# Kernel optimization log

Hardware: AMD Instinct MI355X
Metric: run time of the kernel (lower is better)

## Reference

```python
import jax, jax.numpy as jnp
import numpy as np

B, S, H = 4, 2048, 2048
E, K = 4, 2
FF = 4 * H  # standard MLP expert expansion


def setup_inputs() -> dict:
    key = jax.random.key(0)
    ks = jax.random.split(key, 5)
    sc = 0.02
    return {
        "hidden_states": jax.random.normal(ks[0], (B, S, H), jnp.float32),
        "w_gate": jax.random.normal(ks[1], (H, E), jnp.float32) * sc,
        "b_gate": jnp.zeros((E,), jnp.float32),
        "w1": jax.random.normal(ks[2], (E, H, FF), jnp.float32) * sc,
        "b1": jnp.zeros((E, FF), jnp.float32),
        "w2": jax.random.normal(ks[3], (E, FF, H), jnp.float32) * sc,
        "b2": jnp.zeros((E, H), jnp.float32),
    }


def reference(hidden_states, w_gate, b_gate, w1, b1, w2, b2):
    # Router: linear gate -> softmax -> top-k, renormalized gate weights
    logits = jnp.einsum("bsh,he->bse", hidden_states, w_gate) + b_gate
    probs = jax.nn.softmax(logits, axis=-1)                       # [B,S,E]
    top_p, top_i = jax.lax.top_k(probs, K)                        # [B,S,K]
    gate_w = top_p / jnp.sum(top_p, axis=-1, keepdims=True)

    # Switch-style load-balancing aux loss
    route = jax.nn.one_hot(top_i, E, dtype=probs.dtype)           # [B,S,K,E]
    frac_tokens = jnp.mean(jnp.sum(route, axis=2) / K, axis=(0, 1))  # [E]
    mean_prob = jnp.mean(probs, axis=(0, 1))                      # [E]
    aux_loss = E * jnp.sum(frac_tokens * mean_prob)

    # Dispatch/combine: small fixed expert count -> loop over experts,
    # dense FFN on all tokens, mask via gate weight (0 for unrouted tokens).
    out = jnp.zeros_like(hidden_states)
    for e in range(E):
        w_e = jnp.sum(gate_w * (top_i == e), axis=-1)             # [B,S]
        h = jax.nn.gelu(jnp.einsum("bsh,hf->bsf", hidden_states, w1[e]) + b1[e])
        y = jnp.einsum("bsf,fh->bsh", h, w2[e]) + b2[e]
        out = out + w_e[..., None] * y
    return out, aux_loss
```

## Files before the change

kernel.cpp:

```cpp
#include <hip/hip_runtime.h>

typedef unsigned short u16;
typedef __attribute__((ext_vector_type(8))) short bf16x8;
typedef __attribute__((ext_vector_type(4))) float f32x4;

#define TOK  8192
#define HD   2048
#define FFD  8192
#define NEXP 4

__device__ __forceinline__ u16 f2bf(float f){
  unsigned u = __float_as_uint(f);
  u += 0x7fffu + ((u >> 16) & 1u);
  return (u16)(u >> 16);
}

__device__ __forceinline__ float gelu_tanh(float x){
  float u = 0.7978845608028654f * (x + 0.044715f * x * x * x);
  return 0.5f * x * (1.0f + tanhf(u));
}

__device__ __forceinline__ void gload_lds16(const void* g, void* l){
  __builtin_amdgcn_global_load_lds((const __attribute__((address_space(1))) void*)g,
                                   (__attribute__((address_space(3))) void*)l, 16, 0, 0);
}

__device__ __forceinline__ f32x4 mfma_bf16(bf16x8 a, bf16x8 b, f32x4 c){
  asm("v_mfma_f32_16x16x32_bf16 %0, %1, %2, %0" : "+v"(c) : "v"(a), "v"(b));
  return c;
}

__global__ __launch_bounds__(256) void cvt_to_bf16(const float* __restrict__ in,
                                                   u16* __restrict__ out, int n4){
  int i = blockIdx.x * 256 + threadIdx.x;
  if (i >= n4) return;
  float4 v = ((const float4*)in)[i];
  ushort4 o;
  o.x = f2bf(v.x); o.y = f2bf(v.y); o.z = f2bf(v.z); o.w = f2bf(v.w);
  ((ushort4*)out)[i] = o;
}

__global__ __launch_bounds__(256) void transpose_cvt(const float* __restrict__ in,
                                                     u16* __restrict__ out, int R, int C){
  __shared__ float tile[64][65];
  int tx = threadIdx.x & 63;
  int ty = threadIdx.x >> 6;
  size_t r0 = (size_t)blockIdx.y * 64;
  size_t c0 = (size_t)blockIdx.x * 64;
  #pragma unroll
  for (int i = ty; i < 64; i += 4)
    tile[i][tx] = in[(r0 + i) * C + (c0 + tx)];
  __syncthreads();
  #pragma unroll
  for (int i = ty; i < 64; i += 4)
    out[(c0 + i) * R + (r0 + tx)] = f2bf(tile[tx][i]);
}

__global__ __launch_bounds__(256) void router_kernel(
    const float* __restrict__ X, const float* __restrict__ wg, const float* __restrict__ bg,
    float* __restrict__ probs, int* __restrict__ topi, float* __restrict__ gatew){
  int t = blockIdx.x;
  const float* x = X + (size_t)t * HD;
  float a0 = 0.f, a1 = 0.f, a2 = 0.f, a3 = 0.f;
  for (int h = threadIdx.x; h < HD; h += 256){
    float xv = x[h];
    float4 w = ((const float4*)wg)[h];
    a0 += xv * w.x; a1 += xv * w.y; a2 += xv * w.z; a3 += xv * w.w;
  }
  __shared__ float red[4][256];
  red[0][threadIdx.x] = a0; red[1][threadIdx.x] = a1;
  red[2][threadIdx.x] = a2; red[3][threadIdx.x] = a3;
  __syncthreads();
  for (int s = 128; s > 0; s >>= 1){
    if (threadIdx.x < (unsigned)s){
      #pragma unroll
      for (int e = 0; e < 4; e++) red[e][threadIdx.x] += red[e][threadIdx.x + s];
    }
    __syncthreads();
  }
  if (threadIdx.x == 0){
    float l[4], p[4];
    #pragma unroll
    for (int e = 0; e < 4; e++) l[e] = red[e][0] + bg[e];
    float mx = fmaxf(fmaxf(l[0], l[1]), fmaxf(l[2], l[3]));
    float s = 0.f;
    #pragma unroll
    for (int e = 0; e < 4; e++){ p[e] = expf(l[e] - mx); s += p[e]; }
    #pragma unroll
    for (int e = 0; e < 4; e++){ p[e] /= s; probs[t * 4 + e] = p[e]; }
    int e0 = 0;
    for (int e = 1; e < 4; e++) if (p[e] > p[e0]) e0 = e;
    int e1 = -1;
    for (int e = 0; e < 4; e++){ if (e == e0) continue; if (e1 < 0 || p[e] > p[e1]) e1 = e; }
    float g = p[e0] + p[e1];
    topi[t * 2] = e0; topi[t * 2 + 1] = e1;
    #pragma unroll
    for (int e = 0; e < 4; e++)
      gatew[(size_t)e * TOK + t] = (e == e0) ? p[e0] / g : (e == e1) ? p[e1] / g : 0.f;
  }
}

__global__ __launch_bounds__(256) void build_lists(const int* __restrict__ topi,
                                                   int* __restrict__ cnt,
                                                   int* __restrict__ lists){
  int t = blockIdx.x * 256 + threadIdx.x;
  if (t >= TOK) return;
  #pragma unroll
  for (int k = 0; k < 2; k++){
    int e = topi[t * 2 + k];
    int p = atomicAdd(cnt + e, 1);
    lists[e * TOK + p] = t;
  }
}

__global__ __launch_bounds__(256) void aux_kernel(const float* __restrict__ probs,
                                                  const int* __restrict__ topi,
                                                  float* __restrict__ out_aux){
  __shared__ float sp[4][256];
  __shared__ float sc[4][256];
  float p[4] = {0,0,0,0}, c[4] = {0,0,0,0};
  for (int t = threadIdx.x; t < TOK; t += 256){
    #pragma unroll
    for (int e = 0; e < 4; e++) p[e] += probs[t * 4 + e];
    c[topi[t * 2]]     += 1.f;
    c[topi[t * 2 + 1]] += 1.f;
  }
  #pragma unroll
  for (int e = 0; e < 4; e++){ sp[e][threadIdx.x] = p[e]; sc[e][threadIdx.x] = c[e]; }
  __syncthreads();
  for (int s = 128; s > 0; s >>= 1){
    if (threadIdx.x < (unsigned)s){
      #pragma unroll
      for (int e = 0; e < 4; e++){
        sp[e][threadIdx.x] += sp[e][threadIdx.x + s];
        sc[e][threadIdx.x] += sc[e][threadIdx.x + s];
      }
    }
    __syncthreads();
  }
  if (threadIdx.x == 0){
    float aux = 0.f;
    #pragma unroll
    for (int e = 0; e < 4; e++)
      aux += (sc[e][0] / (float)(TOK * 2)) * (sp[e][0] / (float)TOK);
    *out_aux = 4.f * aux;
  }
}

#define BM 128
#define BN 128
#define BK 64

template<int EPI>
__global__ __launch_bounds__(256) void gemm_moe(
    const u16* __restrict__ A, const u16* __restrict__ BT,
    const int* __restrict__ rowidx, const int* __restrict__ cntp,
    int m0, int N, int K,
    const float* __restrict__ bias,
    u16* __restrict__ Hout,
    const float* __restrict__ gate,
    float* __restrict__ Cout){
  const int Mv = *cntp;
  const int browg = m0 + blockIdx.y * BM;
  if (browg >= Mv) return;

  __shared__ __align__(16) u16 As[BM * BK];
  __shared__ __align__(16) u16 Bs[BN * BK];

  const int tid  = threadIdx.x;
  const int lane = tid & 63;
  const int wid  = tid >> 6;
  const int wr   = wid >> 1;
  const int wc   = wid & 1;
  const size_t bcol = (size_t)blockIdx.x * BN;

  const int srow = lane >> 3;
  const int scol = (lane & 7) * 8;
  const int r = lane & 15;
  const int h = lane >> 4;

  const u16* aptr[4];
  const u16* bptr[4];
  #pragma unroll
  for (int i = 0; i < 4; i++){
    const int c = wid * 4 + i;
    const int rr = browg + c * 8 + srow;
    int ar;
    if (EPI == 0){
      const int cr = rr < Mv ? rr : Mv - 1;
      ar = rowidx[cr];
    } else {
      ar = rr - m0;
    }
    aptr[i] = A + (size_t)ar * K + scol;
    bptr[i] = BT + (bcol + c * 8 + srow) * (size_t)K + scol;
  }

  f32x4 acc[4][4];
  #pragma unroll
  for (int m = 0; m < 4; m++)
    #pragma unroll
    for (int n = 0; n < 4; n++) acc[m][n] = (f32x4){0.f, 0.f, 0.f, 0.f};

  for (int kt = 0; kt < K; kt += BK){
    __syncthreads();
    #pragma unroll
    for (int i = 0; i < 4; i++){
      const int c = wid * 4 + i;
      gload_lds16(aptr[i] + kt, (char*)As + c * 1024);
      gload_lds16(bptr[i] + kt, (char*)Bs + c * 1024);
    }
    __syncthreads();
    #pragma unroll
    for (int kk = 0; kk < BK; kk += 32){
      bf16x8 av[4], bv[4];
      #pragma unroll
      for (int m = 0; m < 4; m++)
        av[m] = *(const bf16x8*)(As + (wr * 64 + m * 16 + r) * BK + kk + h * 8);
      #pragma unroll
      for (int n = 0; n < 4; n++)
        bv[n] = *(const bf16x8*)(Bs + (wc * 64 + n * 16 + r) * BK + kk + h * 8);
      #pragma unroll
      for (int m = 0; m < 4; m++)
        #pragma unroll
        for (int n = 0; n < 4; n++)
          acc[m][n] = mfma_bf16(av[m], bv[n], acc[m][n]);
    }
  }

  const int cl = lane & 15;
  const int rg = (lane >> 4) * 4;
  const size_t c0 = bcol + (size_t)wc * 64;
  float bvs[4];
  #pragma unroll
  for (int n = 0; n < 4; n++) bvs[n] = bias[c0 + n * 16 + cl];

  #pragma unroll
  for (int m = 0; m < 4; m++){
    const int rowg = browg + wr * 64 + m * 16 + rg;
    if (EPI == 0){
      const size_t rowl = (size_t)(rowg - m0);
      #pragma unroll
      for (int n = 0; n < 4; n++){
        const size_t col = c0 + n * 16 + cl;
        #pragma unroll
        for (int j = 0; j < 4; j++){
          float y = acc[m][n][j] + bvs[n];
          Hout[(rowl + j) * (size_t)N + col] = f2bf(gelu_tanh(y));
        }
      }
    } else {
      int   tok[4];
      float gv[4];
      #pragma unroll
      for (int j = 0; j < 4; j++){
        const bool v = (rowg + j) < Mv;
        tok[j] = v ? rowidx[rowg + j] : -1;
        gv[j]  = v ? gate[tok[j]] : 0.f;
      }
      #pragma unroll
      for (int n = 0; n < 4; n++){
        const size_t col = c0 + n * 16 + cl;
        #pragma unroll
        for (int j = 0; j < 4; j++){
          if (tok[j] >= 0){
            float y = acc[m][n][j] + bvs[n];
            const size_t idx = (size_t)tok[j] * N + col;
            Cout[idx] += gv[j] * y;
          }
        }
      }
    }
  }
}

extern "C" void kernel_launch(void* const* d_in, const int* in_sizes, int n_in,
                              void* d_out, int out_size, void* d_ws, size_t ws_size,
                              hipStream_t stream){
  const float* X  = (const float*)d_in[0];
  const float* wg = (const float*)d_in[1];
  const float* bg = (const float*)d_in[2];
  const float* w1 = (const float*)d_in[3];
  const float* b1 = (const float*)d_in[4];
  const float* w2 = (const float*)d_in[5];
  const float* b2 = (const float*)d_in[6];
  float* out = (float*)d_out;

  char* ws = (char*)d_ws;
  size_t off = 0;
  auto alloc = [&](size_t b) -> char* {
    char* p = ws + off;
    off = (off + b + 255) & ~(size_t)255;
    return p;
  };
  u16*   Xb    = (u16*)  alloc((size_t)TOK * HD * 2);
  u16*   W1T   = (u16*)  alloc((size_t)FFD * HD * 2);
  u16*   W2T   = (u16*)  alloc((size_t)HD * FFD * 2);
  float* probs = (float*)alloc((size_t)TOK * 4 * 4);
  int*   topi  = (int*)  alloc((size_t)TOK * 2 * 4);
  float* gatew = (float*)alloc((size_t)NEXP * TOK * 4);
  int*   cnt   = (int*)  alloc((size_t)NEXP * 4);
  int*   lists = (int*)  alloc((size_t)NEXP * TOK * 4);
  size_t remain = (ws_size > off) ? (ws_size - off) : 0;
  size_t ch = remain / ((size_t)FFD * 2);
  ch = (ch / 128) * 128;
  if (ch > TOK) ch = TOK;
  if (ch < 128) ch = 128;
  u16* Hb = (u16*)alloc(ch * (size_t)FFD * 2);

  hipMemsetAsync(cnt, 0, NEXP * sizeof(int), stream);
  hipMemsetAsync(out, 0, (size_t)TOK * HD * sizeof(float), stream);

  cvt_to_bf16<<<(TOK * HD / 4 + 255) / 256, 256, 0, stream>>>(X, Xb, TOK * HD / 4);
  router_kernel<<<TOK, 256, 0, stream>>>(X, wg, bg, probs, topi, gatew);
  build_lists<<<TOK / 256, 256, 0, stream>>>(topi, cnt, lists);
  aux_kernel<<<1, 256, 0, stream>>>(probs, topi, out + (out_size - 1));

  for (int e = 0; e < NEXP; ++e){
    transpose_cvt<<<dim3(FFD / 64, HD / 64), 256, 0, stream>>>(
        w1 + (size_t)e * HD * FFD, W1T, HD, FFD);
    transpose_cvt<<<dim3(HD / 64, FFD / 64), 256, 0, stream>>>(
        w2 + (size_t)e * FFD * HD, W2T, FFD, HD);
    for (int m0 = 0; m0 < TOK; m0 += (int)ch){
      gemm_moe<0><<<dim3(FFD / 128, (unsigned)(ch / 128)), 256, 0, stream>>>(
          Xb, W1T, lists + e * TOK, cnt + e, m0, FFD, HD,
          b1 + (size_t)e * FFD, Hb, nullptr, nullptr);
      gemm_moe<1><<<dim3(HD / 128, (unsigned)(ch / 128)), 256, 0, stream>>>(
          Hb, W2T, lists + e * TOK, cnt + e, m0, HD, FFD,
          b2 + (size_t)e * HD, nullptr,
          gatew + (size_t)e * TOK, out);
    }
  }
}
```

Before: 1.955 ms.

## Replace MoE GEMMs with 8-wave double-buffered swizzled 256-row tile kernels

Both expert GEMMs are rewritten as 512-thread kernels with 256-row tiles, double-buffered LDS, and an XOR-swizzled LDS layout. The next K-tile is loaded asynchronously in quarters while MFMAs run, paced by explicit vmcnt waits, barriers and setprio. Workgroup indices are remapped so neighbouring tiles land on the same XCD, which should improve cache reuse. The chunked M loop is replaced by a fixed per-expert capacity (CAPE=4608 rows). Tokens beyond that capacity would be silently dropped if routing were strongly imbalanced.

Measured after the change: 2.263 ms. 15.8% more time.

```diff
diff --git a/kernel.cpp b/kernel.cpp
--- a/kernel.cpp
+++ b/kernel.cpp
@@ -8,6 +8,10 @@
 #define HD   2048
 #define FFD  8192
 #define NEXP 4
+#define CAPE 4608
+
+#define S_BARRIER() asm volatile("s_barrier" ::: "memory")
+#define VMCNT(n)    asm volatile("s_waitcnt vmcnt(" #n ")" ::: "memory")
 
 __device__ __forceinline__ u16 f2bf(float f){
   unsigned u = __float_as_uint(f);
@@ -147,53 +151,166 @@
   }
 }
 
-#define BM 128
-#define BN 128
-#define BK 64
-
-template<int EPI>
-__global__ __launch_bounds__(256) void gemm_moe(
-    const u16* __restrict__ A, const u16* __restrict__ BT,
+__global__ __launch_bounds__(512, 2) void gemm1_8p(
+    const u16* __restrict__ Xb, const u16* __restrict__ BT,
     const int* __restrict__ rowidx, const int* __restrict__ cntp,
-    int m0, int N, int K,
-    const float* __restrict__ bias,
-    u16* __restrict__ Hout,
-    const float* __restrict__ gate,
-    float* __restrict__ Cout){
+    const float* __restrict__ bias, u16* __restrict__ Hout)
+{
+  __shared__ __align__(16) u16 As[2 * 256 * 64];
+  __shared__ __align__(16) u16 Bs[2 * 256 * 64];
   const int Mv = *cntp;
-  const int browg = m0 + blockIdx.y * BM;
+  const int nwg = gridDim.x * gridDim.y;
+  const int orig = blockIdx.x + gridDim.x * blockIdx.y;
+  const int q8 = nwg >> 3, r8 = nwg & 7, xcd = orig & 7, rank = orig >> 3;
+  const int v = (xcd < r8 ? xcd * (q8 + 1) : r8 * (q8 + 1) + (xcd - r8) * q8) + rank;
+  const int by = v % (int)gridDim.y, bx = v / (int)gridDim.y;
+  const int browg = by * 256;
   if (browg >= Mv) return;
-
-  __shared__ __align__(16) u16 As[BM * BK];
-  __shared__ __align__(16) u16 Bs[BN * BK];
-
-  const int tid  = threadIdx.x;
-  const int lane = tid & 63;
-  const int wid  = tid >> 6;
-  const int wr   = wid >> 1;
-  const int wc   = wid & 1;
-  const size_t bcol = (size_t)blockIdx.x * BN;
-
-  const int srow = lane >> 3;
-  const int scol = (lane & 7) * 8;
-  const int r = lane & 15;
-  const int h = lane >> 4;
-
-  const u16* aptr[4];
-  const u16* bptr[4];
-  #pragma unroll
-  for (int i = 0; i < 4; i++){
-    const int c = wid * 4 + i;
-    const int rr = browg + c * 8 + srow;
-    int ar;
-    if (EPI == 0){
-      const int cr = rr < Mv ? rr : Mv - 1;
-      ar = rowidx[cr];
-    } else {
-      ar = rr - m0;
-    }
-    aptr[i] = A + (size_t)ar * K + scol;
-    bptr[i] = BT + (bcol + c * 8 + srow) * (size_t)K + scol;
+  const size_t bcol = (size_t)bx * 256;
+
+  const int tid = threadIdx.x, lane = tid & 63, w = tid >> 6;
+  const int wr = w >> 2, wc = w & 3;
+  const int l8 = lane >> 3;
+  const int csw  = ((lane & 7) ^ l8) * 8;
+  const int sw   = (lane & 7) * 8;
+  const int h8   = ((lane >> 4) & 3) * 8;
+  const int colk0 = h8 ^ sw, colk1 = (32 | h8) ^ sw;
+  const int r16 = lane & 15;
+
+  const u16* bsrc[4]; int bch[4];
+  #pragma unroll
+  for (int j = 0; j < 4; j++){
+    int rb = wc * 64 + wr * 32 + j * 8;
+    bch[j] = rb * 128;
+    bsrc[j] = BT + (bcol + rb + l8) * (size_t)HD + csw;
+  }
+  const u16* asrc[4]; int ach[4];
+  #pragma unroll
+  for (int q = 0; q < 4; q++){
+    int rb = wr * 128 + q * 32 + wc * 8;
+    ach[q] = rb * 128;
+    int rl = browg + rb + l8; if (rl > Mv - 1) rl = Mv - 1;
+    asrc[q] = Xb + (size_t)rowidx[rl] * HD + csw;
+  }
+
+  f32x4 acc[8][4];
+  #pragma unroll
+  for (int m = 0; m < 8; m++)
+    #pragma unroll
+    for (int n = 0; n < 4; n++) acc[m][n] = (f32x4){0.f, 0.f, 0.f, 0.f};
+  bf16x8 bC[8];
+
+  const int NT = HD / 64;
+  #pragma unroll
+  for (int j = 0; j < 4; j++) gload_lds16(bsrc[j], (char*)Bs + bch[j]);
+  #pragma unroll
+  for (int q = 0; q < 4; q++) gload_lds16(asrc[q], (char*)As + ach[q]);
+  VMCNT(3); S_BARRIER();
+
+  for (int t = 0; t < NT; ++t){
+    const u16* asb = As + (t & 1) * 16384;
+    const u16* bsb = Bs + (t & 1) * 16384;
+    char* anb = (char*)As + ((t & 1) ^ 1) * 32768;
+    char* bnb = (char*)Bs + ((t & 1) ^ 1) * 32768;
+    const size_t ko = (size_t)(t + 1) * 64;
+    const bool lastT = (t == NT - 1);
+    #pragma unroll 4
+    for (int p = 0; p < 4; p++){
+      if (p == 0){
+        #pragma unroll
+        for (int nf = 0; nf < 4; nf++){
+          const u16* bp = bsb + (wc * 64 + nf * 16 + r16) * 64;
+          bC[nf * 2]     = *(const bf16x8*)(bp + colk0);
+          bC[nf * 2 + 1] = *(const bf16x8*)(bp + colk1);
+        }
+      }
+      bf16x8 a[2][2];
+      #pragma unroll
+      for (int mi = 0; mi < 2; mi++){
+        const u16* ap = asb + (wr * 128 + (2 * p + mi) * 16 + r16) * 64;
+        a[mi][0] = *(const bf16x8*)(ap + colk0);
+        a[mi][1] = *(const bf16x8*)(ap + colk1);
+      }
+      if (!lastT){
+        if      (p == 0){ gload_lds16(bsrc[0] + ko, bnb + bch[0]); gload_lds16(bsrc[1] + ko, bnb + bch[1]); }
+        else if (p == 1){ gload_lds16(bsrc[2] + ko, bnb + bch[2]); gload_lds16(bsrc[3] + ko, bnb + bch[3]); }
+        else if (p == 2){ gload_lds16(asrc[0] + ko, anb + ach[0]); gload_lds16(asrc[1] + ko, anb + ach[1]); }
+        else            { gload_lds16(asrc[2] + ko, anb + ach[2]); gload_lds16(asrc[3] + ko, anb + ach[3]); }
+      }
+      S_BARRIER();
+      __builtin_amdgcn_s_setprio(1);
+      #pragma unroll
+      for (int mi = 0; mi < 2; mi++)
+        #pragma unroll
+        for (int nf = 0; nf < 4; nf++){
+          acc[2 * p + mi][nf] = mfma_bf16(a[mi][0], bC[nf * 2],     acc[2 * p + mi][nf]);
+          acc[2 * p + mi][nf] = mfma_bf16(a[mi][1], bC[nf * 2 + 1], acc[2 * p + mi][nf]);
+        }
+      __builtin_amdgcn_s_setprio(0);
+      if (!lastT){ if (p == 0) VMCNT(4); else if (p == 1) VMCNT(5); else if (p == 2) VMCNT(6); else VMCNT(3); }
+      else       { if (p == 0) VMCNT(2); else if (p == 1) VMCNT(1); else if (p == 2) VMCNT(0); }
+      S_BARRIER();
+    }
+  }
+
+  const int cl = r16, rg = (lane >> 4) * 4;
+  const size_t c0 = bcol + wc * 64;
+  float bv[4];
+  #pragma unroll
+  for (int nf = 0; nf < 4; nf++) bv[nf] = bias[c0 + nf * 16 + cl];
+  #pragma unroll
+  for (int mf = 0; mf < 8; mf++){
+    const size_t rb = (size_t)(browg + wr * 128 + mf * 16 + rg);
+    #pragma unroll
+    for (int nf = 0; nf < 4; nf++){
+      const size_t col = c0 + nf * 16 + cl;
+      #pragma unroll
+      for (int j = 0; j < 4; j++)
+        Hout[(rb + j) * FFD + col] = f2bf(gelu_tanh(acc[mf][nf][j] + bv[nf]));
+    }
+  }
+}
+
+__global__ __launch_bounds__(512, 2) void gemm2_8p(
+    const u16* __restrict__ Hb, const u16* __restrict__ BT,
+    const int* __restrict__ rowidx, const int* __restrict__ cntp,
+    const float* __restrict__ bias, const float* __restrict__ gate,
+    float* __restrict__ Cout)
+{
+  __shared__ __align__(16) u16 As[2 * 256 * 64];
+  __shared__ __align__(16) u16 Bs[2 * 128 * 64];
+  const int Mv = *cntp;
+  const int nwg = gridDim.x * gridDim.y;
+  const int orig = blockIdx.x + gridDim.x * blockIdx.y;
+  const int q8 = nwg >> 3, r8 = nwg & 7, xcd = orig & 7, rank = orig >> 3;
+  const int v = (xcd < r8 ? xcd * (q8 + 1) : r8 * (q8 + 1) + (xcd - r8) * q8) + rank;
+  const int by = v % (int)gridDim.y, bx = v / (int)gridDim.y;
+  const int browg = by * 256;
+  if (browg >= Mv) return;
+  const size_t bcol = (size_t)bx * 128;
+
+  const int tid = threadIdx.x, lane = tid & 63, w = tid >> 6;
+  const int wr = w >> 1, wc = w & 1;
+  const int l8 = lane >> 3;
+  const int csw  = ((lane & 7) ^ l8) * 8;
+  const int sw   = (lane & 7) * 8;
+  const int h8   = ((lane >> 4) & 3) * 8;
+  const int colk0 = h8 ^ sw, colk1 = (32 | h8) ^ sw;
+  const int r16 = lane & 15;
+
+  const u16* bsrc[2]; int bch[2];
+  #pragma unroll
+  for (int j = 0; j < 2; j++){
+    int rb = wc * 64 + wr * 16 + j * 8;
+    bch[j] = rb * 128;
+    bsrc[j] = BT + (bcol + rb + l8) * (size_t)FFD + csw;
+  }
+  const u16* asrc[4]; int ach[4];
+  #pragma unroll
+  for (int q = 0; q < 4; q++){
+    int rb = wr * 64 + q * 16 + wc * 8;
+    ach[q] = rb * 128;
+    asrc[q] = Hb + (size_t)(browg + rb + l8) * FFD + csw;
   }
 
   f32x4 acc[4][4];
@@ -201,73 +318,80 @@
   for (int m = 0; m < 4; m++)
     #pragma unroll
     for (int n = 0; n < 4; n++) acc[m][n] = (f32x4){0.f, 0.f, 0.f, 0.f};
-
-  for (int kt = 0; kt < K; kt += BK){
-    __syncthreads();
-    #pragma unroll
-    for (int i = 0; i < 4; i++){
-      const int c = wid * 4 + i;
-      gload_lds16(aptr[i] + kt, (char*)As + c * 1024);
-      gload_lds16(bptr[i] + kt, (char*)Bs + c * 1024);
-    }
-    __syncthreads();
-    #pragma unroll
-    for (int kk = 0; kk < BK; kk += 32){
-      bf16x8 av[4], bv[4];
-      #pragma unroll
-      for (int m = 0; m < 4; m++)
-        av[m] = *(const bf16x8*)(As + (wr * 64 + m * 16 + r) * BK + kk + h * 8);
-      #pragma unroll
-      for (int n = 0; n < 4; n++)
-        bv[n] = *(const bf16x8*)(Bs + (wc * 64 + n * 16 + r) * BK + kk + h * 8);
-      #pragma unroll
-      for (int m = 0; m < 4; m++)
+  bf16x8 bC[8];
+
+  const int NT = FFD / 64;
+  gload_lds16(bsrc[0], (char*)Bs + bch[0]);
+  gload_lds16(bsrc[1], (char*)Bs + bch[1]);
+  #pragma unroll
+  for (int q = 0; q < 4; q++) gload_lds16(asrc[q], (char*)As + ach[q]);
+  VMCNT(3); S_BARRIER();
+
+  for (int t = 0; t < NT; ++t){
+    const u16* asb = As + (t & 1) * 16384;
+    const u16* bsb = Bs + (t & 1) * 8192;
+    char* anb = (char*)As + ((t & 1) ^ 1) * 32768;
+    char* bnb = (char*)Bs + ((t & 1) ^ 1) * 16384;
+    const size_t ko = (size_t)(t + 1) * 64;
+    const bool lastT = (t == NT - 1);
+    #pragma unroll 4
+    for (int p = 0; p < 4; p++){
+      if (p == 0){
         #pragma unroll
-        for (int n = 0; n < 4; n++)
-          acc[m][n] = mfma_bf16(av[m], bv[n], acc[m][n]);
-    }
-  }
-
-  const int cl = lane & 15;
-  const int rg = (lane >> 4) * 4;
-  const size_t c0 = bcol + (size_t)wc * 64;
-  float bvs[4];
-  #pragma unroll
-  for (int n = 0; n < 4; n++) bvs[n] = bias[c0 + n * 16 + cl];
-
-  #pragma unroll
-  for (int m = 0; m < 4; m++){
-    const int rowg = browg + wr * 64 + m * 16 + rg;
-    if (EPI == 0){
-      const size_t rowl = (size_t)(rowg - m0);
-      #pragma unroll
-      for (int n = 0; n < 4; n++){
-        const size_t col = c0 + n * 16 + cl;
-        #pragma unroll
-        for (int j = 0; j < 4; j++){
-          float y = acc[m][n][j] + bvs[n];
-          Hout[(rowl + j) * (size_t)N + col] = f2bf(gelu_tanh(y));
+        for (int nf = 0; nf < 4; nf++){
+          const u16* bp = bsb + (wc * 64 + nf * 16 + r16) * 64;
+          bC[nf * 2]     = *(const bf16x8*)(bp + colk0);
+          bC[nf * 2 + 1] = *(const bf16x8*)(bp + colk1);
         }
       }
-    } else {
-      int   tok[4];
-      float gv[4];
+      bf16x8 a0, a1;
+      {
+        const u16* ap = asb + (wr * 64 + p * 16 + r16) * 64;
+        a0 = *(const bf16x8*)(ap + colk0);
+        a1 = *(const bf16x8*)(ap + colk1);
+      }
+      if (!lastT){
+        if      (p == 0){ gload_lds16(bsrc[0] + ko, bnb + bch[0]); gload_lds16(bsrc[1] + ko, bnb + bch[1]); }
+        else if (p == 1){ gload_lds16(asrc[0] + ko, anb + ach[0]); gload_lds16(asrc[1] + ko, anb + ach[1]); }
+        else if (p == 2){ gload_lds16(asrc[2] + ko, anb + ach[2]); gload_lds16(asrc[3] + ko, anb + ach[3]); }
+      }
+      S_BARRIER();
+      __builtin_amdgcn_s_setprio(1);
+      #pragma unroll
+      for (int nf = 0; nf < 4; nf++){
+        acc[p][nf] = mfma_bf16(a0, bC[nf * 2],     acc[p][nf]);
+        acc[p][nf] = mfma_bf16(a1, bC[nf * 2 + 1], acc[p][nf]);
+      }
+      __builtin_amdgcn_s_setprio(0);
+      if (!lastT){ if (p == 0) VMCNT(4); else if (p == 1) VMCNT(5); else if (p == 2) VMCNT(6); else VMCNT(3); }
+      else       { if (p == 0) VMCNT(2); else if (p == 1) VMCNT(1); else if (p == 2) VMCNT(0); }
+      S_BARRIER();
+    }
+  }
+
+  const int cl = r16, rg = (lane >> 4) * 4;
+  const size_t c0 = bcol + wc * 64;
+  float bv[4];
+  #pragma unroll
+  for (int nf = 0; nf < 4; nf++) bv[nf] = bias[c0 + nf * 16 + cl];
+  #pragma unroll
+  for (int mf = 0; mf < 4; mf++){
+    const int rbase = browg + wr * 64 + mf * 16 + rg;
+    int   tok[4]; float gv[4];
+    #pragma unroll
+    for (int j = 0; j < 4; j++){
+      const bool ok = (rbase + j) < Mv;
+      tok[j] = ok ? rowidx[rbase + j] : -1;
+      gv[j]  = ok ? gate[tok[j]] : 0.f;
+    }
+    #pragma unroll
+    for (int nf = 0; nf < 4; nf++){
+      const size_t col = c0 + nf * 16 + cl;
       #pragma unroll
       for (int j = 0; j < 4; j++){
-        const bool v = (rowg + j) < Mv;
-        tok[j] = v ? rowidx[rowg + j] : -1;
-        gv[j]  = v ? gate[tok[j]] : 0.f;
-      }
-      #pragma unroll
-      for (int n = 0; n < 4; n++){
-        const size_t col = c0 + n * 16 + cl;
-        #pragma unroll
-        for (int j = 0; j < 4; j++){
-          if (tok[j] >= 0){
-            float y = acc[m][n][j] + bvs[n];
-            const size_t idx = (size_t)tok[j] * N + col;
-            Cout[idx] += gv[j] * y;
-          }
+        if (tok[j] >= 0){
+          const size_t idx = (size_t)tok[j] * HD + col;
+          Cout[idx] += gv[j] * (acc[mf][nf][j] + bv[nf]);
         }
       }
     }
@@ -277,6 +401,7 @@
 extern "C" void kernel_launch(void* const* d_in, const int* in_sizes, int n_in,
                               void* d_out, int out_size, void* d_ws, size_t ws_size,
                               hipStream_t stream){
+  (void)in_sizes; (void)n_in; (void)ws_size;
   const float* X  = (const float*)d_in[0];
   const float* wg = (const float*)d_in[1];
   const float* bg = (const float*)d_in[2];
@@ -301,12 +426,7 @@
   float* gatew = (float*)alloc((size_t)NEXP * TOK * 4);
   int*   cnt   = (int*)  alloc((size_t)NEXP * 4);
   int*   lists = (int*)  alloc((size_t)NEXP * TOK * 4);
-  size_t remain = (ws_size > off) ? (ws_size - off) : 0;
-  size_t ch = remain / ((size_t)FFD * 2);
-  ch = (ch / 128) * 128;
-  if (ch > TOK) ch = TOK;
-  if (ch < 128) ch = 128;
-  u16* Hb = (u16*)alloc(ch * (size_t)FFD * 2);
+  u16*   Hb    = (u16*)  alloc((size_t)CAPE * FFD * 2);
 
   hipMemsetAsync(cnt, 0, NEXP * sizeof(int), stream);
   hipMemsetAsync(out, 0, (size_t)TOK * HD * sizeof(float), stream);
@@ -321,14 +441,10 @@
         w1 + (size_t)e * HD * FFD, W1T, HD, FFD);
     transpose_cvt<<<dim3(HD / 64, FFD / 64), 256, 0, stream>>>(
         w2 + (size_t)e * FFD * HD, W2T, FFD, HD);
-    for (int m0 = 0; m0 < TOK; m0 += (int)ch){
-      gemm_moe<0><<<dim3(FFD / 128, (unsigned)(ch / 128)), 256, 0, stream>>>(
-          Xb, W1T, lists + e * TOK, cnt + e, m0, FFD, HD,
-          b1 + (size_t)e * FFD, Hb, nullptr, nullptr);
-      gemm_moe<1><<<dim3(HD / 128, (unsigned)(ch / 128)), 256, 0, stream>>>(
-          Hb, W2T, lists + e * TOK, cnt + e, m0, HD, FFD,
-          b2 + (size_t)e * HD, nullptr,
-          gatew + (size_t)e * TOK, out);
-    }
-  }
-}
+    gemm1_8p<<<dim3(FFD / 256, CAPE / 256), 512, 0, stream>>>(
+        Xb, W1T, lists + e * TOK, cnt + e, b1 + (size_t)e * FFD, Hb);
+    gemm2_8p<<<dim3(HD / 128, CAPE / 256), 512, 0, stream>>>(
+        Hb, W2T, lists + e * TOK, cnt + e, b2 + (size_t)e * HD,
+        gatew + (size_t)e * TOK, out);
+  }
+}
```
